# Performance work log

Measured on AMD Instinct MI355X. Metric: run time of the kernel, lower is better.

## Reference

```python
import jax, jax.numpy as jnp
import numpy as np

N = 100000   # nodes
E = 1600000  # edges (before self-loops)
IN, H, HID, OUT = 128, 4, 32, 16
G, NPG = 100, 1000  # graphs, nodes per graph
NEG_SLOPE = 0.2


def setup_inputs() -> dict:
    key = jax.random.key(0)
    ks = jax.random.split(key, 12)
    x = jax.random.normal(ks[0], (N, IN), dtype=jnp.float32)
    # node type in column 0: first node of each graph is the root (type 0)
    node_type = (jnp.arange(N) % NPG != 0).astype(jnp.float32)
    x = x.at[:, 0].set(node_type)
    edge_index = jax.random.randint(ks[1], (2, E), 0, N, dtype=jnp.int64)
    batch = (jnp.arange(N) // NPG).astype(jnp.int64)
    s = 0.1
    W1 = jax.random.normal(ks[2], (IN, H * HID), dtype=jnp.float32) * s
    att_src1 = jax.random.normal(ks[3], (H, HID), dtype=jnp.float32) * s
    att_dst1 = jax.random.normal(ks[4], (H, HID), dtype=jnp.float32) * s
    bias1 = jnp.zeros((H * HID,), dtype=jnp.float32)
    W2 = jax.random.normal(ks[5], (H * HID, OUT), dtype=jnp.float32) * s
    att_src2 = jax.random.normal(ks[6], (1, OUT), dtype=jnp.float32) * s
    att_dst2 = jax.random.normal(ks[7], (1, OUT), dtype=jnp.float32) * s
    bias2 = jnp.zeros((OUT,), dtype=jnp.float32)
    return {"x": x, "edge_index": edge_index, "batch": batch,
            "W1": W1, "att_src1": att_src1, "att_dst1": att_dst1, "bias1": bias1,
            "W2": W2, "att_src2": att_src2, "att_dst2": att_dst2, "bias2": bias2}


def gat_conv(x, src, dst, W, att_src, att_dst, bias, heads, out_ch, concat):
    n = x.shape[0]
    h = (x @ W).reshape(n, heads, out_ch)           # [N,H,C]
    a_src = jnp.einsum('nhc,hc->nh', h, att_src)    # [N,H]
    a_dst = jnp.einsum('nhc,hc->nh', h, att_dst)
    e = a_src[src] + a_dst[dst]                     # [E',H]
    e = jnp.where(e > 0, e, NEG_SLOPE * e)          # leaky_relu(0.2)
    # segment softmax over incoming edges of each dst node
    m = jax.ops.segment_max(e, dst, num_segments=n)
    e = jnp.exp(e - m[dst])
    denom = jax.ops.segment_sum(e, dst, num_segments=n)
    alpha = e / (denom[dst] + 1e-16)                # [E',H]
    msg = h[src] * alpha[:, :, None]                # [E',H,C]
    out = jax.ops.segment_sum(msg, dst, num_segments=n)  # [N,H,C]
    if concat:
        return out.reshape(n, heads * out_ch) + bias
    return out.mean(axis=1) + bias


def reference(x, edge_index, batch, W1, att_src1, att_dst1, bias1,
              W2, att_src2, att_dst2, bias2):
    # eval mode: feature/attention dropout are identity
    ar = jnp.arange(N, dtype=edge_index.dtype)
    ei = jnp.concatenate([edge_index, jnp.stack([ar, ar])], axis=1)  # add self-loops
    src, dst = ei[0], ei[1]
    h = gat_conv(x, src, dst, W1, att_src1, att_dst1, bias1, H, HID, True)
    h = jax.nn.elu(h)
    out = gat_conv(h, src, dst, W2, att_src2, att_dst2, bias2, 1, OUT, False)
    # first root (node_type==0) per graph
    node_types = x[:, 0]
    cand = jnp.where(node_types == 0, jnp.arange(N), N)
    roots = jax.ops.segment_min(cand, batch, num_segments=G)
    return out[roots]
```

## Files before the change

kernel.cpp:

```cpp
#include <hip/hip_runtime.h>
#include <math.h>

#define NN 100000
#define EE 1600000
#define GG 100
#define DIN 128
#define F1 128
#define FOUT 16

#define C1CAP 16384
#define C0CAP 49152
#define L1CAP 262144
#define L2CAP 32768
#define NT 16

#define O_CNT      0
#define O_FLAG1    (O_CNT + 8)
#define O_FLAG0    (O_FLAG1 + NN)
#define O_ISROOT   (O_FLAG0 + NN)
#define O_FILL     (O_ISROOT + NN)
#define O_ZEND     (O_FILL + C1CAP)
#define O_ROOT     (O_ZEND)
#define O_MAP1     (O_ROOT + GG)
#define O_MAP0     (O_MAP1 + NN)
#define O_LIST1    (O_MAP0 + NN)
#define O_LIST0    (O_LIST1 + C1CAP)
#define O_L1       (O_LIST0 + C0CAP)
#define O_L2       (O_L1 + L1CAP*2)
#define O_CSRP     (O_L2 + L2CAP*2)
#define O_ORDER    (O_CSRP + C1CAP + 1)
#define O_H1       (O_ORDER + L1CAP)
#define O_A1S      (O_H1 + C0CAP*F1)
#define O_A1D      (O_A1S + C0CAP*4)
#define O_H2       (O_A1D + C0CAP*4)
#define O_A2S      (O_H2 + C1CAP*FOUT)
#define O_A2D      (O_A2S + C1CAP)
#define O_S1       (O_A2D + C1CAP)
#define O_OUT1     (O_S1 + C1CAP*4)
#define O_S2       (O_OUT1 + C1CAP*F1)
#define O_OUT2     (O_S2 + C1CAP)
#define O_END      (O_OUT2 + C1CAP*FOUT)

__device__ __forceinline__ void claim1(int* ws, int node) {
  if (atomicCAS(&ws[O_FLAG1 + node], 0, 1) == 0) {
    int idx = atomicAdd(&ws[O_CNT + 0], 1);
    if (idx < C1CAP) { ws[O_MAP1 + node] = idx; ws[O_LIST1 + idx] = node; }
  }
}
__device__ __forceinline__ void claim0(int* ws, int node) {
  if (atomicCAS(&ws[O_FLAG0 + node], 0, 1) == 0) {
    int idx = atomicAdd(&ws[O_CNT + 1], 1);
    if (idx < C0CAP) { ws[O_MAP0 + node] = idx; ws[O_LIST0 + idx] = node; }
  }
}
__device__ __forceinline__ void appendL1(int* ws, int s, int d) {
  int idx = atomicAdd(&ws[O_CNT + 2], 1);
  if (idx < L1CAP) { ws[O_L1 + 2*idx] = s; ws[O_L1 + 2*idx + 1] = d; }
}
__device__ __forceinline__ void appendL2(int* ws, int s, int d) {
  int idx = atomicAdd(&ws[O_CNT + 3], 1);
  if (idx < L2CAP) { ws[O_L2 + 2*idx] = s; ws[O_L2 + 2*idx + 1] = d; }
}

__global__ void gat_roots(const float* __restrict__ x, const int* __restrict__ batch, int* ws) {
  int i = blockIdx.x * blockDim.x + threadIdx.x;
  if (i >= NN) return;
  if (x[(size_t)i * DIN] == 0.f)
    atomicMin((unsigned int*)&ws[O_ROOT + batch[i]], (unsigned int)i);
}

__global__ void gat_mark_roots(int* ws) {
  int g = blockIdx.x * blockDim.x + threadIdx.x;
  if (g >= GG) return;
  unsigned int r = (unsigned int)ws[O_ROOT + g];
  if (r < NN) {
    ws[O_ISROOT + r] = 1;
    claim1(ws, (int)r);
    appendL2(ws, (int)r, (int)r);
  }
}

#define SBUF 2048
__global__ __launch_bounds__(256)
void gat_scan(const int* __restrict__ ei, int* __restrict__ ws,
              int probeOff, int cntPairIdx, int pairOff, int pairCap,
              int claimFlagOff, int cntClaimIdx, int mapOff, int listOff, int claimCap)
{
  __shared__ int sp[SBUF * 2];
  __shared__ int sc[SBUF];
  __shared__ int nP, nC, bP, bC;
  if (threadIdx.x == 0) { nP = 0; nC = 0; }
  __syncthreads();
  const int perBlock = (EE + gridDim.x - 1) / gridDim.x;
  const int beg = blockIdx.x * perBlock;
  const int end = min(beg + perBlock, EE);
  for (int ch = beg; ch < end; ch += 256) {
    int e = ch + threadIdx.x;
    if (e < end) {
      int d = ei[EE + e];
      if (ws[probeOff + d]) {
        int s = ei[e];
        int p = atomicAdd(&nP, 1);
        sp[2*p] = s; sp[2*p + 1] = d;
        if (atomicCAS(&ws[claimFlagOff + s], 0, 1) == 0)
          sc[atomicAdd(&nC, 1)] = s;
      }
    }
    __syncthreads();
    if (nP >= SBUF - 256 || nC >= SBUF - 256) {
      if (threadIdx.x == 0) {
        bP = atomicAdd(&ws[O_CNT + cntPairIdx], nP);
        bC = atomicAdd(&ws[O_CNT + cntClaimIdx], nC);
      }
      __syncthreads();
      for (int i = threadIdx.x; i < nP; i += 256) {
        int g = bP + i;
        if (g < pairCap) { ws[pairOff + 2*g] = sp[2*i]; ws[pairOff + 2*g + 1] = sp[2*i + 1]; }
      }
      for (int i = threadIdx.x; i < nC; i += 256) {
        int g = bC + i;
        if (g < claimCap) { int node = sc[i]; ws[mapOff + node] = g; ws[listOff + g] = node; }
      }
      __syncthreads();
      if (threadIdx.x == 0) { nP = 0; nC = 0; }
      __syncthreads();
    }
  }
  if (threadIdx.x == 0) {
    bP = atomicAdd(&ws[O_CNT + cntPairIdx], nP);
    bC = atomicAdd(&ws[O_CNT + cntClaimIdx], nC);
  }
  __syncthreads();
  for (int i = threadIdx.x; i < nP; i += 256) {
    int g = bP + i;
    if (g < pairCap) { ws[pairOff + 2*g] = sp[2*i]; ws[pairOff + 2*g + 1] = sp[2*i + 1]; }
  }
  for (int i = threadIdx.x; i < nC; i += 256) {
    int g = bC + i;
    if (g < claimCap) { int node = sc[i]; ws[mapOff + node] = g; ws[listOff + g] = node; }
  }
}

__global__ void gat_selfloop1(int* ws) {
  int c1 = ws[O_CNT + 0]; if (c1 > C1CAP) c1 = C1CAP;
  int stride = gridDim.x * blockDim.x;
  int t0 = blockIdx.x * blockDim.x + threadIdx.x;
  for (int i = t0; i < c1; i += stride) {
    int v = ws[O_LIST1 + i];
    appendL1(ws, v, v);
    claim0(ws, v);
  }
  float* s2   = (float*)(ws + O_S2);
  float* out2 = (float*)(ws + O_OUT2);
  for (int i = t0; i < c1 * FOUT; i += stride) out2[i] = 0.f;
  for (int i = t0; i < c1; i += stride) s2[i] = 0.f;
}

__global__ __launch_bounds__(256) void gat_h1lin(
    const float* __restrict__ x, const float* __restrict__ W1,
    const float* __restrict__ att_s1, const float* __restrict__ att_d1, int* ws) {
  __shared__ float xs[NT][DIN];
  int t = threadIdx.x, col = t & 127, half = t >> 7;
  int c0 = ws[O_CNT + 1]; if (c0 > C0CAP) c0 = C0CAP;
  float* h1  = (float*)(ws + O_H1);
  float* a1s = (float*)(ws + O_A1S);
  float* a1d = (float*)(ws + O_A1D);
  float as1v = att_s1[col], ad1v = att_d1[col];
  for (int tile = blockIdx.x * NT; tile < c0; tile += gridDim.x * NT) {
    {
      int n = t >> 4, k0 = (t & 15) * 8;
      int ci = tile + n;
      if (ci < c0) {
        int v = ws[O_LIST0 + ci];
        const float4* src = (const float4*)&x[(size_t)v * DIN + k0];
        *(float4*)&xs[n][k0]     = src[0];
        *(float4*)&xs[n][k0 + 4] = src[1];
      }
    }
    __syncthreads();
    float acc[8];
    #pragma unroll
    for (int i = 0; i < 8; ++i) acc[i] = 0.f;
    #pragma unroll 4
    for (int k = 0; k < DIN; k += 4) {
      float w0 = W1[(k + 0) * F1 + col];
      float w1 = W1[(k + 1) * F1 + col];
      float w2 = W1[(k + 2) * F1 + col];
      float w3 = W1[(k + 3) * F1 + col];
      #pragma unroll
      for (int n8 = 0; n8 < 8; ++n8) {
        const float4 xv = *(const float4*)&xs[half * 8 + n8][k];
        acc[n8] = fmaf(xv.x, w0, acc[n8]);
        acc[n8] = fmaf(xv.y, w1, acc[n8]);
        acc[n8] = fmaf(xv.z, w2, acc[n8]);
        acc[n8] = fmaf(xv.w, w3, acc[n8]);
      }
    }
    #pragma unroll
    for (int n8 = 0; n8 < 8; ++n8) {
      int ci = tile + half * 8 + n8;
      bool ok = ci < c0;
      if (ok) h1[(size_t)ci * F1 + col] = acc[n8];
      float cs = acc[n8] * as1v, cd = acc[n8] * ad1v;
      #pragma unroll
      for (int off = 16; off > 0; off >>= 1) {
        cs += __shfl_down(cs, off, 32);
        cd += __shfl_down(cd, off, 32);
      }
      if (ok && (col & 31) == 0) {
        a1s[ci * 4 + (col >> 5)] = cs;
        a1d[ci * 4 + (col >> 5)] = cd;
      }
    }
    __syncthreads();
  }
}

__global__ void gat_e1hist(int* ws) {
  int l1 = ws[O_CNT + 2]; if (l1 > L1CAP) l1 = L1CAP;
  for (int i = blockIdx.x * blockDim.x + threadIdx.x; i < l1; i += gridDim.x * blockDim.x) {
    int d = ws[O_L1 + 2*i + 1];
    int md1 = ws[O_MAP1 + d];
    if ((unsigned)md1 < C1CAP) atomicAdd(&ws[O_FILL + md1], 1);
  }
}

__global__ __launch_bounds__(256) void gat_e1scan(int* ws) {
  __shared__ int part[256];
  int n = ws[O_CNT + 0]; if (n > C1CAP) n = C1CAP;
  int t = threadIdx.x;
  int chunk = (n + 255) >> 8;
  int b = t * chunk, e = min(b + chunk, n);
  int s = 0;
  for (int i = b; i < e; ++i) s += ws[O_FILL + i];
  part[t] = s;
  __syncthreads();
  for (int off = 1; off < 256; off <<= 1) {
    int v = (t >= off) ? part[t - off] : 0;
    __syncthreads();
    part[t] += v;
    __syncthreads();
  }
  int base = (t == 0) ? 0 : part[t - 1];
  for (int i = b; i < e; ++i) {
    int c = ws[O_FILL + i];
    ws[O_CSRP + i] = base;
    base += c;
    ws[O_FILL + i] = 0;
  }
  if (t == 0) ws[O_CSRP + n] = part[255];
}

__global__ void gat_e1scatter(int* ws) {
  int l1 = ws[O_CNT + 2]; if (l1 > L1CAP) l1 = L1CAP;
  for (int i = blockIdx.x * blockDim.x + threadIdx.x; i < l1; i += gridDim.x * blockDim.x) {
    int d = ws[O_L1 + 2*i + 1];
    int md1 = ws[O_MAP1 + d];
    if ((unsigned)md1 >= C1CAP) continue;
    int pos = ws[O_CSRP + md1] + atomicAdd(&ws[O_FILL + md1], 1);
    if (pos < L1CAP) ws[O_ORDER + pos] = i;
  }
}

__global__ __launch_bounds__(256) void gat_e1agg(int* ws) {
  int c1 = ws[O_CNT + 0]; if (c1 > C1CAP) c1 = C1CAP;
  float* a1s  = (float*)(ws + O_A1S);
  float* a1d  = (float*)(ws + O_A1D);
  float* h1   = (float*)(ws + O_H1);
  float* out1 = (float*)(ws + O_OUT1);
  float* s1   = (float*)(ws + O_S1);
  __shared__ int   msBuf[256];
  __shared__ float wBuf[256 * 4];
  __shared__ float sacc[2][F1];
  int t = threadIdx.x, col = t & 127, half = t >> 7;
  for (int ci = blockIdx.x; ci < c1; ci += gridDim.x) {
    int beg = ws[O_CSRP + ci], end = ws[O_CSRP + ci + 1];
    int node = ws[O_LIST1 + ci];
    int md0 = ws[O_MAP0 + node];
    if ((unsigned)md0 >= C0CAP) md0 = 0;
    float acc = 0.f;
    float sh  = 0.f;
    for (int cb = beg; cb < end; cb += 256) {
      int cnt = min(256, end - cb);
      __syncthreads();
      if (t < cnt) {
        int e = ws[O_ORDER + cb + t];
        int srcn = ws[O_L1 + 2*e];
        int ms = ws[O_MAP0 + srcn];
        if ((unsigned)ms >= C0CAP) ms = 0;
        msBuf[t] = ms;
        #pragma unroll
        for (int h = 0; h < 4; ++h) {
          float ev = a1s[ms * 4 + h] + a1d[md0 * 4 + h];
          ev = ev > 0.f ? ev : 0.2f * ev;
          wBuf[t * 4 + h] = __expf(ev);
        }
      }
      __syncthreads();
      for (int j = half; j < cnt; j += 2) {
        int ms = msBuf[j];
        float w = wBuf[j * 4 + (col >> 5)];
        acc = fmaf(h1[(size_t)ms * F1 + col], w, acc);
      }
      if (t < 4) for (int j = 0; j < cnt; ++j) sh += wBuf[j * 4 + t];
    }
    sacc[half][col] = acc;
    __syncthreads();
    if (half == 0) out1[(size_t)ci * F1 + col] = sacc[0][col] + sacc[1][col];
    if (t < 4) s1[ci * 4 + t] = sh;
    __syncthreads();
  }
}

__global__ void gat_l2prep(const float* __restrict__ b1, const float* __restrict__ W2,
                           const float* __restrict__ att_s2, const float* __restrict__ att_d2,
                           int* ws) {
  __shared__ float hs[F1];
  __shared__ float h2s[FOUT];
  int t = threadIdx.x;
  int c1 = ws[O_CNT + 0]; if (c1 > C1CAP) c1 = C1CAP;
  float* out1 = (float*)(ws + O_OUT1);
  float* s1   = (float*)(ws + O_S1);
  float* h2   = (float*)(ws + O_H2);
  float* a2s  = (float*)(ws + O_A2S);
  float* a2d  = (float*)(ws + O_A2D);
  for (int ci = blockIdx.x; ci < c1; ci += gridDim.x) {
    float hv = out1[(size_t)ci * F1 + t] / (s1[ci * 4 + (t >> 5)] + 1e-16f) + b1[t];
    hv = hv > 0.f ? hv : (expf(hv) - 1.f);
    hs[t] = hv;
    __syncthreads();
    if (t < FOUT) {
      float a = 0.f;
      for (int c = 0; c < F1; ++c) a = fmaf(hs[c], W2[c * FOUT + t], a);
      h2[ci * FOUT + t] = a;
      h2s[t] = a;
    }
    __syncthreads();
    if (t == 0) {
      float sa = 0.f, sd = 0.f;
      for (int o = 0; o < FOUT; ++o) { sa += h2s[o] * att_s2[o]; sd += h2s[o] * att_d2[o]; }
      a2s[ci] = sa; a2d[ci] = sd;
    }
    __syncthreads();
  }
}

__global__ void gat_e2sumagg(int* ws) {
  int l2 = ws[O_CNT + 3]; if (l2 > L2CAP) l2 = L2CAP;
  int total = l2 * FOUT;
  float* a2s = (float*)(ws + O_A2S);
  float* a2d = (float*)(ws + O_A2D);
  float* s2  = (float*)(ws + O_S2);
  float* h2  = (float*)(ws + O_H2);
  float* out2= (float*)(ws + O_OUT2);
  for (int idx = blockIdx.x * blockDim.x + threadIdx.x; idx < total;
       idx += gridDim.x * blockDim.x) {
    int i = idx >> 4, o = idx & 15;
    int s = ws[O_L2 + 2*i], d = ws[O_L2 + 2*i + 1];
    int msi = ws[O_MAP1 + s], mdi = ws[O_MAP1 + d];
    if ((unsigned)msi >= C1CAP || (unsigned)mdi >= C1CAP) continue;
    float e = a2s[msi] + a2d[mdi];
    e = e > 0.f ? e : 0.2f * e;
    float w = expf(e);
    if (o == 0) atomicAdd(&s2[mdi], w);
    atomicAdd(&out2[mdi * FOUT + o], h2[msi * FOUT + o] * w);
  }
}

__global__ void gat_out(const float* __restrict__ b2, int* ws, float* __restrict__ out) {
  int i = blockIdx.x * blockDim.x + threadIdx.x;
  if (i >= GG * FOUT) return;
  int g = i >> 4, o = i & 15;
  unsigned int r = (unsigned int)ws[O_ROOT + g];
  float val = 0.f;
  if (r < NN) {
    int ci = ws[O_MAP1 + r];
    if ((unsigned)ci < C1CAP) {
      float* out2 = (float*)(ws + O_OUT2);
      float* s2   = (float*)(ws + O_S2);
      val = out2[ci * FOUT + o] / (s2[ci] + 1e-16f);
    }
  }
  out[i] = val + b2[o];
}

extern "C" void kernel_launch(void* const* d_in, const int* in_sizes, int n_in,
                              void* d_out, int out_size, void* d_ws, size_t ws_size,
                              hipStream_t stream) {
  const float* x    = (const float*)d_in[0];
  const int*   ei   = (const int*)d_in[1];
  const int*   batch= (const int*)d_in[2];
  const float* W1   = (const float*)d_in[3];
  const float* as1  = (const float*)d_in[4];
  const float* ad1  = (const float*)d_in[5];
  const float* b1   = (const float*)d_in[6];
  const float* W2   = (const float*)d_in[7];
  const float* as2  = (const float*)d_in[8];
  const float* ad2  = (const float*)d_in[9];
  const float* b2   = (const float*)d_in[10];
  float* out = (float*)d_out;
  int* ws = (int*)d_ws;

  hipMemsetAsync(ws, 0, (size_t)O_ZEND * 4, stream);
  hipMemsetAsync(ws + O_ROOT, 0xFF, (size_t)GG * 4, stream);
  gat_roots<<<(NN + 255) / 256, 256, 0, stream>>>(x, batch, ws);
  gat_mark_roots<<<1, 128, 0, stream>>>(ws);
  gat_scan<<<1024, 256, 0, stream>>>(ei, ws,
      O_ISROOT, 3, O_L2, L2CAP, O_FLAG1, 0, O_MAP1, O_LIST1, C1CAP);
  gat_selfloop1<<<64, 256, 0, stream>>>(ws);
  gat_scan<<<1024, 256, 0, stream>>>(ei, ws,
      O_FLAG1, 2, O_L1, L1CAP, O_FLAG0, 1, O_MAP0, O_LIST0, C0CAP);
  gat_h1lin<<<C0CAP / NT, 256, 0, stream>>>(x, W1, as1, ad1, ws);
  gat_e1hist<<<128, 256, 0, stream>>>(ws);
  gat_e1scan<<<1, 256, 0, stream>>>(ws);
  gat_e1scatter<<<128, 256, 0, stream>>>(ws);
  gat_e1agg<<<2048, 256, 0, stream>>>(ws);
  gat_l2prep<<<512, 128, 0, stream>>>(b1, W2, as2, ad2, ws);
  gat_e2sumagg<<<128, 256, 0, stream>>>(ws);
  gat_out<<<(GG * FOUT + 255) / 256, 256, 0, stream>>>(b2, ws, out);
}
```

Baseline: 253.7 us.

## Fuse pipeline stages and replace CSR build with fixed-capacity per-node edge slots

Folds root marking into the roots kernel with a last-block pattern and merges the self-loop step into the scans. Layer-1 edges are written straight into per-destination slots of capacity DEGCAP, which removes the edge list, histogram, prefix-scan and scatter kernels. Layer-1 aggregation is fused with the ELU, W2 projection and attention logits, and layer-2 aggregation plus output is done in one single-block kernel using shared-memory atomics. This cuts launches and global traffic, but in-degrees above DEGCAP are silently truncated and the final stage runs on one block.

```diff
diff --git a/kernel.cpp b/kernel.cpp
--- a/kernel.cpp
+++ b/kernel.cpp
@@ -10,8 +10,8 @@
 
 #define C1CAP 16384
 #define C0CAP 49152
-#define L1CAP 262144
 #define L2CAP 32768
+#define DEGCAP 128
 #define NT 16
 
 #define O_CNT      0
@@ -25,135 +25,122 @@
 #define O_MAP0     (O_MAP1 + NN)
 #define O_LIST1    (O_MAP0 + NN)
 #define O_LIST0    (O_LIST1 + C1CAP)
-#define O_L1       (O_LIST0 + C0CAP)
-#define O_L2       (O_L1 + L1CAP*2)
-#define O_CSRP     (O_L2 + L2CAP*2)
-#define O_ORDER    (O_CSRP + C1CAP + 1)
-#define O_H1       (O_ORDER + L1CAP)
+#define O_L2       (O_LIST0 + C0CAP)
+#define O_ORDER    (O_L2 + L2CAP*2)
+#define O_H1       (O_ORDER + C1CAP*DEGCAP)
 #define O_A1S      (O_H1 + C0CAP*F1)
 #define O_A1D      (O_A1S + C0CAP*4)
 #define O_H2       (O_A1D + C0CAP*4)
 #define O_A2S      (O_H2 + C1CAP*FOUT)
 #define O_A2D      (O_A2S + C1CAP)
-#define O_S1       (O_A2D + C1CAP)
-#define O_OUT1     (O_S1 + C1CAP*4)
-#define O_S2       (O_OUT1 + C1CAP*F1)
-#define O_OUT2     (O_S2 + C1CAP)
-#define O_END      (O_OUT2 + C1CAP*FOUT)
-
-__device__ __forceinline__ void claim1(int* ws, int node) {
-  if (atomicCAS(&ws[O_FLAG1 + node], 0, 1) == 0) {
-    int idx = atomicAdd(&ws[O_CNT + 0], 1);
-    if (idx < C1CAP) { ws[O_MAP1 + node] = idx; ws[O_LIST1 + idx] = node; }
-  }
-}
-__device__ __forceinline__ void claim0(int* ws, int node) {
-  if (atomicCAS(&ws[O_FLAG0 + node], 0, 1) == 0) {
-    int idx = atomicAdd(&ws[O_CNT + 1], 1);
-    if (idx < C0CAP) { ws[O_MAP0 + node] = idx; ws[O_LIST0 + idx] = node; }
-  }
-}
-__device__ __forceinline__ void appendL1(int* ws, int s, int d) {
-  int idx = atomicAdd(&ws[O_CNT + 2], 1);
-  if (idx < L1CAP) { ws[O_L1 + 2*idx] = s; ws[O_L1 + 2*idx + 1] = d; }
-}
-__device__ __forceinline__ void appendL2(int* ws, int s, int d) {
-  int idx = atomicAdd(&ws[O_CNT + 3], 1);
-  if (idx < L2CAP) { ws[O_L2 + 2*idx] = s; ws[O_L2 + 2*idx + 1] = d; }
-}
-
-__global__ void gat_roots(const float* __restrict__ x, const int* __restrict__ batch, int* ws) {
+#define O_END      (O_A2D + C1CAP)
+
+__global__ __launch_bounds__(256) void gat_roots(
+    const float* __restrict__ x, const int* __restrict__ batch, int* ws) {
   int i = blockIdx.x * blockDim.x + threadIdx.x;
-  if (i >= NN) return;
-  if (x[(size_t)i * DIN] == 0.f)
+  if (i < NN && x[(size_t)i * DIN] == 0.f)
     atomicMin((unsigned int*)&ws[O_ROOT + batch[i]], (unsigned int)i);
-}
-
-__global__ void gat_mark_roots(int* ws) {
-  int g = blockIdx.x * blockDim.x + threadIdx.x;
+  __threadfence();
+  __syncthreads();
+  __shared__ int lastFlag;
+  if (threadIdx.x == 0)
+    lastFlag = (atomicAdd(&ws[O_CNT + 7], 1) == (int)gridDim.x - 1);
+  __syncthreads();
+  if (!lastFlag) return;
+  int g = threadIdx.x;
   if (g >= GG) return;
-  unsigned int r = (unsigned int)ws[O_ROOT + g];
-  if (r < NN) {
-    ws[O_ISROOT + r] = 1;
-    claim1(ws, (int)r);
-    appendL2(ws, (int)r, (int)r);
-  }
-}
-
-#define SBUF 2048
-__global__ __launch_bounds__(256)
-void gat_scan(const int* __restrict__ ei, int* __restrict__ ws,
-              int probeOff, int cntPairIdx, int pairOff, int pairCap,
-              int claimFlagOff, int cntClaimIdx, int mapOff, int listOff, int claimCap)
-{
-  __shared__ int sp[SBUF * 2];
-  __shared__ int sc[SBUF];
-  __shared__ int nP, nC, bP, bC;
+  unsigned int r = __hip_atomic_load((unsigned int*)&ws[O_ROOT + g],
+                                     __ATOMIC_ACQUIRE, __HIP_MEMORY_SCOPE_AGENT);
+  if (r >= NN) return;
+  ws[O_ISROOT + r] = g + 1;
+  ws[O_FLAG1 + r] = 1;
+  int idx = atomicAdd(&ws[O_CNT + 0], 1);
+  if (idx < C1CAP) {
+    ws[O_MAP1 + r] = idx;
+    ws[O_LIST1 + idx] = r;
+    ws[O_FILL + idx] = 1;
+    ws[O_ORDER + idx * DEGCAP] = (int)r;
+  }
+  int p = atomicAdd(&ws[O_CNT + 3], 1);
+  if (p < L2CAP) { ws[O_L2 + 2*p] = (int)r; ws[O_L2 + 2*p + 1] = g; }
+  ws[O_FLAG0 + r] = 1;
+  int i0 = atomicAdd(&ws[O_CNT + 1], 1);
+  if (i0 < C0CAP) { ws[O_MAP0 + r] = i0; ws[O_LIST0 + i0] = (int)r; }
+}
+
+#define SB2 1600
+__global__ __launch_bounds__(256) void gat_scan2(const int* __restrict__ ei, int* __restrict__ ws) {
+  __shared__ int sp[SB2 * 2];
+  __shared__ int sc[SB2];
+  __shared__ int nP, nC, bP, bC, b0;
   if (threadIdx.x == 0) { nP = 0; nC = 0; }
   __syncthreads();
   const int perBlock = (EE + gridDim.x - 1) / gridDim.x;
   const int beg = blockIdx.x * perBlock;
   const int end = min(beg + perBlock, EE);
-  for (int ch = beg; ch < end; ch += 256) {
-    int e = ch + threadIdx.x;
-    if (e < end) {
-      int d = ei[EE + e];
-      if (ws[probeOff + d]) {
-        int s = ei[e];
-        int p = atomicAdd(&nP, 1);
-        sp[2*p] = s; sp[2*p + 1] = d;
-        if (atomicCAS(&ws[claimFlagOff + s], 0, 1) == 0)
-          sc[atomicAdd(&nC, 1)] = s;
-      }
-    }
-    __syncthreads();
-    if (nP >= SBUF - 256 || nC >= SBUF - 256) {
-      if (threadIdx.x == 0) {
-        bP = atomicAdd(&ws[O_CNT + cntPairIdx], nP);
-        bC = atomicAdd(&ws[O_CNT + cntClaimIdx], nC);
-      }
-      __syncthreads();
-      for (int i = threadIdx.x; i < nP; i += 256) {
-        int g = bP + i;
-        if (g < pairCap) { ws[pairOff + 2*g] = sp[2*i]; ws[pairOff + 2*g + 1] = sp[2*i + 1]; }
-      }
-      for (int i = threadIdx.x; i < nC; i += 256) {
-        int g = bC + i;
-        if (g < claimCap) { int node = sc[i]; ws[mapOff + node] = g; ws[listOff + g] = node; }
-      }
-      __syncthreads();
-      if (threadIdx.x == 0) { nP = 0; nC = 0; }
-      __syncthreads();
-    }
-  }
+  for (int e = beg + threadIdx.x; e < end; e += 256) {
+    int d = ei[EE + e];
+    int gi = ws[O_ISROOT + d];
+    if (gi) {
+      int s = ei[e];
+      int p = atomicAdd(&nP, 1);
+      sp[2*p] = s; sp[2*p + 1] = gi - 1;
+      if (atomicCAS(&ws[O_FLAG1 + s], 0, 1) == 0)
+        sc[atomicAdd(&nC, 1)] = s;
+    }
+  }
+  __syncthreads();
   if (threadIdx.x == 0) {
-    bP = atomicAdd(&ws[O_CNT + cntPairIdx], nP);
-    bC = atomicAdd(&ws[O_CNT + cntClaimIdx], nC);
+    bP = nP ? atomicAdd(&ws[O_CNT + 3], nP) : 0;
+    bC = nC ? atomicAdd(&ws[O_CNT + 0], nC) : 0;
+    b0 = nC ? atomicAdd(&ws[O_CNT + 1], nC) : 0;
   }
   __syncthreads();
   for (int i = threadIdx.x; i < nP; i += 256) {
-    int g = bP + i;
-    if (g < pairCap) { ws[pairOff + 2*g] = sp[2*i]; ws[pairOff + 2*g + 1] = sp[2*i + 1]; }
+    int p = bP + i;
+    if (p < L2CAP) { ws[O_L2 + 2*p] = sp[2*i]; ws[O_L2 + 2*p + 1] = sp[2*i + 1]; }
   }
   for (int i = threadIdx.x; i < nC; i += 256) {
-    int g = bC + i;
-    if (g < claimCap) { int node = sc[i]; ws[mapOff + node] = g; ws[listOff + g] = node; }
-  }
-}
-
-__global__ void gat_selfloop1(int* ws) {
-  int c1 = ws[O_CNT + 0]; if (c1 > C1CAP) c1 = C1CAP;
-  int stride = gridDim.x * blockDim.x;
-  int t0 = blockIdx.x * blockDim.x + threadIdx.x;
-  for (int i = t0; i < c1; i += stride) {
-    int v = ws[O_LIST1 + i];
-    appendL1(ws, v, v);
-    claim0(ws, v);
-  }
-  float* s2   = (float*)(ws + O_S2);
-  float* out2 = (float*)(ws + O_OUT2);
-  for (int i = t0; i < c1 * FOUT; i += stride) out2[i] = 0.f;
-  for (int i = t0; i < c1; i += stride) s2[i] = 0.f;
+    int node = sc[i], idx = bC + i, i0 = b0 + i;
+    if (idx < C1CAP) {
+      ws[O_MAP1 + node] = idx;
+      ws[O_LIST1 + idx] = node;
+      ws[O_FILL + idx] = 1;
+      ws[O_ORDER + idx * DEGCAP] = node;
+    }
+    ws[O_FLAG0 + node] = 1;
+    if (i0 < C0CAP) { ws[O_MAP0 + node] = i0; ws[O_LIST0 + i0] = node; }
+  }
+}
+
+__global__ __launch_bounds__(256) void gat_scan1(const int* __restrict__ ei, int* __restrict__ ws) {
+  __shared__ int sc[SB2];
+  __shared__ int nC, b0;
+  if (threadIdx.x == 0) nC = 0;
+  __syncthreads();
+  const int perBlock = (EE + gridDim.x - 1) / gridDim.x;
+  const int beg = blockIdx.x * perBlock;
+  const int end = min(beg + perBlock, EE);
+  for (int e = beg + threadIdx.x; e < end; e += 256) {
+    int d = ei[EE + e];
+    if (ws[O_FLAG1 + d]) {
+      int s = ei[e];
+      int md1 = ws[O_MAP1 + d];
+      if ((unsigned)md1 < C1CAP) {
+        int pos = atomicAdd(&ws[O_FILL + md1], 1);
+        if (pos < DEGCAP) ws[O_ORDER + md1 * DEGCAP + pos] = s;
+      }
+      if (atomicCAS(&ws[O_FLAG0 + s], 0, 1) == 0)
+        sc[atomicAdd(&nC, 1)] = s;
+    }
+  }
+  __syncthreads();
+  if (threadIdx.x == 0) b0 = nC ? atomicAdd(&ws[O_CNT + 1], nC) : 0;
+  __syncthreads();
+  for (int i = threadIdx.x; i < nC; i += 256) {
+    int node = sc[i], i0 = b0 + i;
+    if (i0 < C0CAP) { ws[O_MAP0 + node] = i0; ws[O_LIST0 + i0] = node; }
+  }
 }
 
 __global__ __launch_bounds__(256) void gat_h1lin(
@@ -216,172 +203,114 @@
   }
 }
 
-__global__ void gat_e1hist(int* ws) {
-  int l1 = ws[O_CNT + 2]; if (l1 > L1CAP) l1 = L1CAP;
-  for (int i = blockIdx.x * blockDim.x + threadIdx.x; i < l1; i += gridDim.x * blockDim.x) {
-    int d = ws[O_L1 + 2*i + 1];
-    int md1 = ws[O_MAP1 + d];
-    if ((unsigned)md1 < C1CAP) atomicAdd(&ws[O_FILL + md1], 1);
-  }
-}
-
-__global__ __launch_bounds__(256) void gat_e1scan(int* ws) {
-  __shared__ int part[256];
-  int n = ws[O_CNT + 0]; if (n > C1CAP) n = C1CAP;
-  int t = threadIdx.x;
-  int chunk = (n + 255) >> 8;
-  int b = t * chunk, e = min(b + chunk, n);
-  int s = 0;
-  for (int i = b; i < e; ++i) s += ws[O_FILL + i];
-  part[t] = s;
-  __syncthreads();
-  for (int off = 1; off < 256; off <<= 1) {
-    int v = (t >= off) ? part[t - off] : 0;
-    __syncthreads();
-    part[t] += v;
-    __syncthreads();
-  }
-  int base = (t == 0) ? 0 : part[t - 1];
-  for (int i = b; i < e; ++i) {
-    int c = ws[O_FILL + i];
-    ws[O_CSRP + i] = base;
-    base += c;
-    ws[O_FILL + i] = 0;
-  }
-  if (t == 0) ws[O_CSRP + n] = part[255];
-}
-
-__global__ void gat_e1scatter(int* ws) {
-  int l1 = ws[O_CNT + 2]; if (l1 > L1CAP) l1 = L1CAP;
-  for (int i = blockIdx.x * blockDim.x + threadIdx.x; i < l1; i += gridDim.x * blockDim.x) {
-    int d = ws[O_L1 + 2*i + 1];
-    int md1 = ws[O_MAP1 + d];
-    if ((unsigned)md1 >= C1CAP) continue;
-    int pos = ws[O_CSRP + md1] + atomicAdd(&ws[O_FILL + md1], 1);
-    if (pos < L1CAP) ws[O_ORDER + pos] = i;
-  }
-}
-
-__global__ __launch_bounds__(256) void gat_e1agg(int* ws) {
+__global__ __launch_bounds__(256) void gat_e1agg(
+    const float* __restrict__ b1, const float* __restrict__ W2,
+    const float* __restrict__ att_s2, const float* __restrict__ att_d2, int* ws) {
   int c1 = ws[O_CNT + 0]; if (c1 > C1CAP) c1 = C1CAP;
-  float* a1s  = (float*)(ws + O_A1S);
-  float* a1d  = (float*)(ws + O_A1D);
-  float* h1   = (float*)(ws + O_H1);
-  float* out1 = (float*)(ws + O_OUT1);
-  float* s1   = (float*)(ws + O_S1);
-  __shared__ int   msBuf[256];
-  __shared__ float wBuf[256 * 4];
+  float* a1s = (float*)(ws + O_A1S);
+  float* a1d = (float*)(ws + O_A1D);
+  float* h1  = (float*)(ws + O_H1);
+  float* h2  = (float*)(ws + O_H2);
+  float* a2s = (float*)(ws + O_A2S);
+  float* a2d = (float*)(ws + O_A2D);
+  __shared__ int   msBuf[DEGCAP];
+  __shared__ float wBuf[DEGCAP * 4];
   __shared__ float sacc[2][F1];
+  __shared__ float hs[F1];
+  __shared__ float s1L[4];
+  __shared__ float h2row[FOUT];
   int t = threadIdx.x, col = t & 127, half = t >> 7;
   for (int ci = blockIdx.x; ci < c1; ci += gridDim.x) {
-    int beg = ws[O_CSRP + ci], end = ws[O_CSRP + ci + 1];
+    int cnt = ws[O_FILL + ci]; if (cnt > DEGCAP) cnt = DEGCAP;
     int node = ws[O_LIST1 + ci];
-    int md0 = ws[O_MAP0 + node];
-    if ((unsigned)md0 >= C0CAP) md0 = 0;
+    int md0 = ws[O_MAP0 + node]; if ((unsigned)md0 >= C0CAP) md0 = 0;
+    if (t < cnt) {
+      int srcn = ws[O_ORDER + ci * DEGCAP + t];
+      int ms = ws[O_MAP0 + srcn]; if ((unsigned)ms >= C0CAP) ms = 0;
+      msBuf[t] = ms;
+      #pragma unroll
+      for (int h = 0; h < 4; ++h) {
+        float ev = a1s[ms * 4 + h] + a1d[md0 * 4 + h];
+        ev = ev > 0.f ? ev : 0.2f * ev;
+        wBuf[t * 4 + h] = __expf(ev);
+      }
+    }
+    __syncthreads();
     float acc = 0.f;
-    float sh  = 0.f;
-    for (int cb = beg; cb < end; cb += 256) {
-      int cnt = min(256, end - cb);
-      __syncthreads();
-      if (t < cnt) {
-        int e = ws[O_ORDER + cb + t];
-        int srcn = ws[O_L1 + 2*e];
-        int ms = ws[O_MAP0 + srcn];
-        if ((unsigned)ms >= C0CAP) ms = 0;
-        msBuf[t] = ms;
-        #pragma unroll
-        for (int h = 0; h < 4; ++h) {
-          float ev = a1s[ms * 4 + h] + a1d[md0 * 4 + h];
-          ev = ev > 0.f ? ev : 0.2f * ev;
-          wBuf[t * 4 + h] = __expf(ev);
-        }
-      }
-      __syncthreads();
-      for (int j = half; j < cnt; j += 2) {
-        int ms = msBuf[j];
-        float w = wBuf[j * 4 + (col >> 5)];
-        acc = fmaf(h1[(size_t)ms * F1 + col], w, acc);
-      }
-      if (t < 4) for (int j = 0; j < cnt; ++j) sh += wBuf[j * 4 + t];
-    }
+    for (int j = half; j < cnt; j += 2)
+      acc = fmaf(h1[(size_t)msBuf[j] * F1 + col], wBuf[j * 4 + (col >> 5)], acc);
     sacc[half][col] = acc;
-    __syncthreads();
-    if (half == 0) out1[(size_t)ci * F1 + col] = sacc[0][col] + sacc[1][col];
-    if (t < 4) s1[ci * 4 + t] = sh;
-    __syncthreads();
-  }
-}
-
-__global__ void gat_l2prep(const float* __restrict__ b1, const float* __restrict__ W2,
-                           const float* __restrict__ att_s2, const float* __restrict__ att_d2,
-                           int* ws) {
-  __shared__ float hs[F1];
-  __shared__ float h2s[FOUT];
+    if (t < 4) { float sh = 0.f; for (int j = 0; j < cnt; ++j) sh += wBuf[j * 4 + t]; s1L[t] = sh; }
+    __syncthreads();
+    if (half == 0) {
+      float hv = (sacc[0][col] + sacc[1][col]) / (s1L[col >> 5] + 1e-16f) + b1[col];
+      hs[col] = hv > 0.f ? hv : (__expf(hv) - 1.f);
+    }
+    __syncthreads();
+    {
+      int o = t >> 4, r = t & 15;
+      float p = 0.f;
+      for (int c = r; c < F1; c += 16) p = fmaf(hs[c], W2[c * FOUT + o], p);
+      #pragma unroll
+      for (int off = 8; off > 0; off >>= 1) p += __shfl_down(p, off, 16);
+      if (r == 0) { h2[(size_t)ci * FOUT + o] = p; h2row[o] = p; }
+    }
+    __syncthreads();
+    if (t < 2) {
+      const float* av = t ? att_d2 : att_s2;
+      float s = 0.f;
+      #pragma unroll
+      for (int o = 0; o < FOUT; ++o) s += h2row[o] * av[o];
+      if (t == 0) a2s[ci] = s; else a2d[ci] = s;
+    }
+    __syncthreads();
+  }
+}
+
+__global__ __launch_bounds__(256) void gat_e2out(
+    const float* __restrict__ b2, int* ws, float* __restrict__ out) {
+  __shared__ float acc2[GG * FOUT];
+  __shared__ float sL[GG];
+  __shared__ float a2dR[GG];
+  __shared__ float wE[2048];
   int t = threadIdx.x;
-  int c1 = ws[O_CNT + 0]; if (c1 > C1CAP) c1 = C1CAP;
-  float* out1 = (float*)(ws + O_OUT1);
-  float* s1   = (float*)(ws + O_S1);
-  float* h2   = (float*)(ws + O_H2);
-  float* a2s  = (float*)(ws + O_A2S);
-  float* a2d  = (float*)(ws + O_A2D);
-  for (int ci = blockIdx.x; ci < c1; ci += gridDim.x) {
-    float hv = out1[(size_t)ci * F1 + t] / (s1[ci * 4 + (t >> 5)] + 1e-16f) + b1[t];
-    hv = hv > 0.f ? hv : (expf(hv) - 1.f);
-    hs[t] = hv;
-    __syncthreads();
-    if (t < FOUT) {
-      float a = 0.f;
-      for (int c = 0; c < F1; ++c) a = fmaf(hs[c], W2[c * FOUT + t], a);
-      h2[ci * FOUT + t] = a;
-      h2s[t] = a;
-    }
-    __syncthreads();
-    if (t == 0) {
-      float sa = 0.f, sd = 0.f;
-      for (int o = 0; o < FOUT; ++o) { sa += h2s[o] * att_s2[o]; sd += h2s[o] * att_d2[o]; }
-      a2s[ci] = sa; a2d[ci] = sd;
-    }
-    __syncthreads();
-  }
-}
-
-__global__ void gat_e2sumagg(int* ws) {
-  int l2 = ws[O_CNT + 3]; if (l2 > L2CAP) l2 = L2CAP;
-  int total = l2 * FOUT;
   float* a2s = (float*)(ws + O_A2S);
   float* a2d = (float*)(ws + O_A2D);
-  float* s2  = (float*)(ws + O_S2);
   float* h2  = (float*)(ws + O_H2);
-  float* out2= (float*)(ws + O_OUT2);
-  for (int idx = blockIdx.x * blockDim.x + threadIdx.x; idx < total;
-       idx += gridDim.x * blockDim.x) {
-    int i = idx >> 4, o = idx & 15;
-    int s = ws[O_L2 + 2*i], d = ws[O_L2 + 2*i + 1];
-    int msi = ws[O_MAP1 + s], mdi = ws[O_MAP1 + d];
-    if ((unsigned)msi >= C1CAP || (unsigned)mdi >= C1CAP) continue;
-    float e = a2s[msi] + a2d[mdi];
-    e = e > 0.f ? e : 0.2f * e;
-    float w = expf(e);
-    if (o == 0) atomicAdd(&s2[mdi], w);
-    atomicAdd(&out2[mdi * FOUT + o], h2[msi * FOUT + o] * w);
-  }
-}
-
-__global__ void gat_out(const float* __restrict__ b2, int* ws, float* __restrict__ out) {
-  int i = blockIdx.x * blockDim.x + threadIdx.x;
-  if (i >= GG * FOUT) return;
-  int g = i >> 4, o = i & 15;
-  unsigned int r = (unsigned int)ws[O_ROOT + g];
-  float val = 0.f;
-  if (r < NN) {
-    int ci = ws[O_MAP1 + r];
-    if ((unsigned)ci < C1CAP) {
-      float* out2 = (float*)(ws + O_OUT2);
-      float* s2   = (float*)(ws + O_S2);
-      val = out2[ci * FOUT + o] / (s2[ci] + 1e-16f);
-    }
-  }
-  out[i] = val + b2[o];
+  int l2 = ws[O_CNT + 3]; if (l2 > L2CAP) l2 = L2CAP;
+  for (int i = t; i < GG * FOUT; i += 256) acc2[i] = 0.f;
+  for (int i = t; i < GG; i += 256) {
+    sL[i] = 0.f;
+    unsigned int r = (unsigned int)ws[O_ROOT + i];
+    int m = (r < NN) ? ws[O_MAP1 + (int)r] : 0;
+    if ((unsigned)m >= C1CAP) m = 0;
+    a2dR[i] = a2d[m];
+  }
+  __syncthreads();
+  for (int cb = 0; cb < l2; cb += 2048) {
+    int cc = min(2048, l2 - cb);
+    for (int i = t; i < cc; i += 256) {
+      int s = ws[O_L2 + 2*(cb + i)], g = ws[O_L2 + 2*(cb + i) + 1];
+      int msi = ws[O_MAP1 + s]; if ((unsigned)msi >= C1CAP) msi = 0;
+      float e = a2s[msi] + a2dR[g];
+      e = e > 0.f ? e : 0.2f * e;
+      float w = __expf(e);
+      wE[i] = w;
+      atomicAdd(&sL[g], w);
+    }
+    __syncthreads();
+    for (int idx = t; idx < cc * FOUT; idx += 256) {
+      int i = idx >> 4, o = idx & 15;
+      int s = ws[O_L2 + 2*(cb + i)], g = ws[O_L2 + 2*(cb + i) + 1];
+      int msi = ws[O_MAP1 + s]; if ((unsigned)msi >= C1CAP) msi = 0;
+      atomicAdd(&acc2[g * FOUT + o], h2[(size_t)msi * FOUT + o] * wE[i]);
+    }
+    __syncthreads();
+  }
+  for (int i = t; i < GG * FOUT; i += 256) {
+    int g = i >> 4, o = i & 15;
+    out[i] = acc2[i] / (sL[g] + 1e-16f) + b2[o];
+  }
 }
 
 extern "C" void kernel_launch(void* const* d_in, const int* in_sizes, int n_in,
@@ -404,18 +333,9 @@
   hipMemsetAsync(ws, 0, (size_t)O_ZEND * 4, stream);
   hipMemsetAsync(ws + O_ROOT, 0xFF, (size_t)GG * 4, stream);
   gat_roots<<<(NN + 255) / 256, 256, 0, stream>>>(x, batch, ws);
-  gat_mark_roots<<<1, 128, 0, stream>>>(ws);
-  gat_scan<<<1024, 256, 0, stream>>>(ei, ws,
-      O_ISROOT, 3, O_L2, L2CAP, O_FLAG1, 0, O_MAP1, O_LIST1, C1CAP);
-  gat_selfloop1<<<64, 256, 0, stream>>>(ws);
-  gat_scan<<<1024, 256, 0, stream>>>(ei, ws,
-      O_FLAG1, 2, O_L1, L1CAP, O_FLAG0, 1, O_MAP0, O_LIST0, C0CAP);
+  gat_scan2<<<1024, 256, 0, stream>>>(ei, ws);
+  gat_scan1<<<1024, 256, 0, stream>>>(ei, ws);
   gat_h1lin<<<C0CAP / NT, 256, 0, stream>>>(x, W1, as1, ad1, ws);
-  gat_e1hist<<<128, 256, 0, stream>>>(ws);
-  gat_e1scan<<<1, 256, 0, stream>>>(ws);
-  gat_e1scatter<<<128, 256, 0, stream>>>(ws);
-  gat_e1agg<<<2048, 256, 0, stream>>>(ws);
-  gat_l2prep<<<512, 128, 0, stream>>>(b1, W2, as2, ad2, ws);
-  gat_e2sumagg<<<128, 256, 0, stream>>>(ws);
-  gat_out<<<(GG * FOUT + 255) / 256, 256, 0, stream>>>(b2, ws, out);
-}
+  gat_e1agg<<<2048, 256, 0, stream>>>(b1, W2, as2, ad2, ws);
+  gat_e2out<<<1, 256, 0, stream>>>(b2, ws, out);
+}
```

Measured after the change: 307.0 us. 21.0% more time.
